# Kernel optimization log

Measured on AMD Instinct MI355X. Metric: run time of the kernel, lower is better.

The kernel has to match this reference:

```python
import jax, jax.numpy as jnp
import numpy as np


def setup_inputs() -> dict:
    key = jax.random.key(0)
    k1, k2, k3, k4 = jax.random.split(key, 4)
    B, S, IN, H = 4, 2048, 512, 1024
    x = jax.random.normal(k1, (B, S, IN), dtype=jnp.float32)
    W1 = jax.random.normal(k2, (IN, H), dtype=jnp.float32) * (1.0 / np.sqrt(IN))
    b1 = jax.random.normal(k3, (H,), dtype=jnp.float32) * 0.02
    Wq = jax.random.normal(k4, (H, H), dtype=jnp.float32) * (1.0 / np.sqrt(H))
    return {"x": x, "W1": W1, "b1": b1, "Wq": Wq, "atten_size": 16}


def reference(x, W1, b1, Wq, atten_size):
    A = atten_size
    B, S, _ = x.shape
    H = W1.shape[1]
    h = jax.nn.relu(jnp.einsum('bsi,ih->bsh', x, W1) + b1)  # [B,S,H]
    # zero-pad sequence dim by A on each side
    padded = jnp.pad(h, ((0, 0), (A, A), (0, 0)))  # [B,S+2A,H]
    # torch: stack(roll(padded, k, 1) for k in -A..A, dim=2) then slice [A:-A]
    # => x_nei[b, i, j] = padded[b, 2A + i - j]
    idx = 2 * A + jnp.arange(S)[:, None] - jnp.arange(2 * A + 1)[None, :]  # [S,W]
    x_nei = padded[:, idx, :]  # [B,S,W,H]
    q = jnp.einsum('bsh,hk->bsk', h, Wq)  # [B,S,H]
    scores = jnp.einsum('bsh,bswh->bsw', q, x_nei) / jnp.sqrt(jnp.asarray(H, x.dtype))
    w = jax.nn.softmax(scores, axis=2)  # softmax over window axis
    out = jnp.einsum('bsw,bswh->bsh', w, x_nei)
    return out
```

## Files before the change

kernel.cpp:

```cpp
#include <hip/hip_runtime.h>
#include <stdint.h>

constexpr int BATCH = 4;
constexpr int SEQ   = 2048;
constexpr int DIN   = 512;
constexpr int DH    = 1024;
constexpr int BS    = BATCH * SEQ;
constexpr int AP    = 32;
constexpr int AW    = 64;

typedef float  floatx4 __attribute__((ext_vector_type(4)));
typedef short  bf16x8  __attribute__((ext_vector_type(8)));

static __device__ __forceinline__ unsigned short f2bf(float f) {
  union { float f; unsigned u; } v; v.f = f;
  unsigned r = (v.u + 0x7fffu + ((v.u >> 16) & 1u)) >> 16;
  return (unsigned short)r;
}

static __device__ __forceinline__ void gld_lds16(const unsigned short* g, const short* l) {
  typedef const __attribute__((address_space(1))) void* gvp;
  typedef __attribute__((address_space(3))) void* lvp;
  __builtin_amdgcn_global_load_lds((gvp)(uintptr_t)g, (lvp)(unsigned)(uintptr_t)l, 16, 0, 0);
}

__global__ __launch_bounds__(256) void transpose_w_k(const float* __restrict__ W1,
                                                     const float* __restrict__ Wq,
                                                     unsigned short* __restrict__ w1t,
                                                     unsigned short* __restrict__ wqt) {
  __shared__ float t[32][33];
  const bool isW1 = blockIdx.y < 16;
  const float* in = isW1 ? W1 : Wq;
  unsigned short* out = isW1 ? w1t : wqt;
  const int R = isW1 ? DIN : DH;
  const int C = DH;
  const int r0 = (isW1 ? blockIdx.y : (blockIdx.y - 16)) * 32;
  const int c0 = blockIdx.x * 32;
  const int tx = threadIdx.x & 31, ty = threadIdx.x >> 5;
  for (int i = ty; i < 32; i += 8) t[i][tx] = in[(size_t)(r0 + i) * C + c0 + tx];
  __syncthreads();
  for (int i = ty; i < 32; i += 8) out[(size_t)(c0 + i) * R + r0 + tx] = f2bf(t[tx][i]);
}

__global__ __launch_bounds__(256) void gemm1_k(const float* __restrict__ X,
                                               const unsigned short* __restrict__ Bt,
                                               const float* __restrict__ bias,
                                               unsigned short* __restrict__ outB,
                                               unsigned short* __restrict__ outBT) {
  const int M = BS, N = DH, K = DIN;
  __shared__ __align__(16) short As0[128 * 32], As1[128 * 32];
  __shared__ __align__(16) short Bs0[128 * 32], Bs1[128 * 32];
  const int tid  = threadIdx.x;
  const int m0   = blockIdx.x * 128, n0 = blockIdx.y * 128;
  const int wv   = tid >> 6, lane = tid & 63;
  const int wm   = (wv >> 1) * 64, wn = (wv & 1) * 64;
  const int l16  = lane & 15, quad = lane >> 4;

  const int ar = tid >> 1, acol = (tid & 1) * 16;
  const float* gX = X + (size_t)(m0 + ar) * K + acol;
  short* lA0 = &As0[ar * 32 + acol];
  short* lA1 = &As1[ar * 32 + acol];
  const int ra = lane >> 2, ca = (lane & 3) * 8;
  const unsigned short* gB = Bt + (size_t)(n0 + wv * 32 + ra) * K + ca;
  const short* lB0a = &Bs0[wv * 1024];
  const short* lB0b = &Bs0[wv * 1024 + 512];
  const short* lB1a = &Bs1[wv * 1024];
  const short* lB1b = &Bs1[wv * 1024 + 512];

  floatx4 acc[4][4];
  for (int i = 0; i < 4; i++)
    for (int j = 0; j < 4; j++) acc[i][j] = {0.f, 0.f, 0.f, 0.f};

  for (int ks = 0; ks < K / 64; ++ks) {
    float4 x0 = ((const float4*)gX)[0], x1 = ((const float4*)gX)[1];
    float4 x2 = ((const float4*)gX)[2], x3 = ((const float4*)gX)[3];
    float4 x4 = ((const float4*)(gX + 32))[0], x5 = ((const float4*)(gX + 32))[1];
    float4 x6 = ((const float4*)(gX + 32))[2], x7 = ((const float4*)(gX + 32))[3];
    gX += 64;
    __align__(16) unsigned short c0[16], c1[16];
    c0[0] = f2bf(x0.x); c0[1] = f2bf(x0.y); c0[2]  = f2bf(x0.z); c0[3]  = f2bf(x0.w);
    c0[4] = f2bf(x1.x); c0[5] = f2bf(x1.y); c0[6]  = f2bf(x1.z); c0[7]  = f2bf(x1.w);
    c0[8] = f2bf(x2.x); c0[9] = f2bf(x2.y); c0[10] = f2bf(x2.z); c0[11] = f2bf(x2.w);
    c0[12] = f2bf(x3.x); c0[13] = f2bf(x3.y); c0[14] = f2bf(x3.z); c0[15] = f2bf(x3.w);
    c1[0] = f2bf(x4.x); c1[1] = f2bf(x4.y); c1[2]  = f2bf(x4.z); c1[3]  = f2bf(x4.w);
    c1[4] = f2bf(x5.x); c1[5] = f2bf(x5.y); c1[6]  = f2bf(x5.z); c1[7]  = f2bf(x5.w);
    c1[8] = f2bf(x6.x); c1[9] = f2bf(x6.y); c1[10] = f2bf(x6.z); c1[11] = f2bf(x6.w);
    c1[12] = f2bf(x7.x); c1[13] = f2bf(x7.y); c1[14] = f2bf(x7.z); c1[15] = f2bf(x7.w);
    __syncthreads();
    gld_lds16(gB, lB0a); gld_lds16(gB + 16 * K, lB0b);
    gld_lds16(gB + 32, lB1a); gld_lds16(gB + 16 * K + 32, lB1b);
    gB += 64;
    ((uint4*)lA0)[0] = ((uint4*)c0)[0];
    ((uint4*)lA0)[1] = ((uint4*)c0)[1];
    ((uint4*)lA1)[0] = ((uint4*)c1)[0];
    ((uint4*)lA1)[1] = ((uint4*)c1)[1];
    __syncthreads();
    bf16x8 af[4], bfr[4];
    for (int i = 0; i < 4; i++)
      af[i] = *(const bf16x8*)&As0[(wm + i * 16 + l16) * 32 + quad * 8];
    for (int j = 0; j < 4; j++)
      bfr[j] = *(const bf16x8*)&Bs0[(wn + j * 16 + l16) * 32 + quad * 8];
    for (int i = 0; i < 4; i++)
      for (int j = 0; j < 4; j++)
        acc[i][j] = __builtin_amdgcn_mfma_f32_16x16x32_bf16(af[i], bfr[j], acc[i][j], 0, 0, 0);
    for (int i = 0; i < 4; i++)
      af[i] = *(const bf16x8*)&As1[(wm + i * 16 + l16) * 32 + quad * 8];
    for (int j = 0; j < 4; j++)
      bfr[j] = *(const bf16x8*)&Bs1[(wn + j * 16 + l16) * 32 + quad * 8];
    for (int i = 0; i < 4; i++)
      for (int j = 0; j < 4; j++)
        acc[i][j] = __builtin_amdgcn_mfma_f32_16x16x32_bf16(af[i], bfr[j], acc[i][j], 0, 0, 0);
  }

  for (int j = 0; j < 4; j++) {
    const int col = n0 + wn + j * 16 + l16;
    const float bv = bias[col];
    for (int i = 0; i < 4; i++) {
      const int rowb = m0 + wm + i * 16 + quad * 4;
      float v[4];
      for (int r = 0; r < 4; r++) v[r] = fmaxf(acc[i][j][r] + bv, 0.f);
      for (int r = 0; r < 4; r++) outB[(size_t)(rowb + r) * N + col] = f2bf(v[r]);
      ushort4 o4; o4.x = f2bf(v[0]); o4.y = f2bf(v[1]); o4.z = f2bf(v[2]); o4.w = f2bf(v[3]);
      *(ushort4*)(outBT + (size_t)col * M + rowb) = o4;
    }
  }
}

__global__ __launch_bounds__(256) void gemm2_k(const unsigned short* __restrict__ Ab,
                                               const unsigned short* __restrict__ Bt,
                                               unsigned short* __restrict__ outB) {
  const int N = DH, K = DH;
  __shared__ __align__(16) short As0[128 * 32], As1[128 * 32];
  __shared__ __align__(16) short Bs0[128 * 32], Bs1[128 * 32];
  const int tid  = threadIdx.x;
  const int m0   = blockIdx.x * 128, n0 = blockIdx.y * 128;
  const int wv   = tid >> 6, lane = tid & 63;
  const int wm   = (wv >> 1) * 64, wn = (wv & 1) * 64;
  const int l16  = lane & 15, quad = lane >> 4;

  const int ra = lane >> 2, ca = (lane & 3) * 8;
  const unsigned short* gA = Ab + (size_t)(m0 + wv * 32 + ra) * K + ca;
  const unsigned short* gB = Bt + (size_t)(n0 + wv * 32 + ra) * K + ca;
  const short* lA0a = &As0[wv * 1024];
  const short* lA0b = &As0[wv * 1024 + 512];
  const short* lA1a = &As1[wv * 1024];
  const short* lA1b = &As1[wv * 1024 + 512];
  const short* lB0a = &Bs0[wv * 1024];
  const short* lB0b = &Bs0[wv * 1024 + 512];
  const short* lB1a = &Bs1[wv * 1024];
  const short* lB1b = &Bs1[wv * 1024 + 512];

  floatx4 acc[4][4];
  for (int i = 0; i < 4; i++)
    for (int j = 0; j < 4; j++) acc[i][j] = {0.f, 0.f, 0.f, 0.f};

  for (int ks = 0; ks < K / 64; ++ks) {
    __syncthreads();
    gld_lds16(gA, lA0a); gld_lds16(gA + 16 * K, lA0b);
    gld_lds16(gA + 32, lA1a); gld_lds16(gA + 16 * K + 32, lA1b);
    gld_lds16(gB, lB0a); gld_lds16(gB + 16 * K, lB0b);
    gld_lds16(gB + 32, lB1a); gld_lds16(gB + 16 * K + 32, lB1b);
    gA += 64; gB += 64;
    __syncthreads();
    bf16x8 af[4], bfr[4];
    for (int i = 0; i < 4; i++)
      af[i] = *(const bf16x8*)&As0[(wm + i * 16 + l16) * 32 + quad * 8];
    for (int j = 0; j < 4; j++)
      bfr[j] = *(const bf16x8*)&Bs0[(wn + j * 16 + l16) * 32 + quad * 8];
    for (int i = 0; i < 4; i++)
      for (int j = 0; j < 4; j++)
        acc[i][j] = __builtin_amdgcn_mfma_f32_16x16x32_bf16(af[i], bfr[j], acc[i][j], 0, 0, 0);
    for (int i = 0; i < 4; i++)
      af[i] = *(const bf16x8*)&As1[(wm + i * 16 + l16) * 32 + quad * 8];
    for (int j = 0; j < 4; j++)
      bfr[j] = *(const bf16x8*)&Bs1[(wn + j * 16 + l16) * 32 + quad * 8];
    for (int i = 0; i < 4; i++)
      for (int j = 0; j < 4; j++)
        acc[i][j] = __builtin_amdgcn_mfma_f32_16x16x32_bf16(af[i], bfr[j], acc[i][j], 0, 0, 0);
  }

  for (int j = 0; j < 4; j++) {
    const int col = n0 + wn + j * 16 + l16;
    for (int i = 0; i < 4; i++) {
      const int rowb = m0 + wm + i * 16 + quad * 4;
      for (int r = 0; r < 4; r++)
        outB[(size_t)(rowb + r) * N + col] = f2bf(acc[i][j][r]);
    }
  }
}

__global__ __launch_bounds__(512) void attn_mfma_k(const unsigned short* __restrict__ hb,
                                                   const unsigned short* __restrict__ hbT,
                                                   const unsigned short* __restrict__ qb,
                                                   float* __restrict__ out) {
  __shared__ float Sf[32 * 64];
  __shared__ __align__(16) short Ps[32 * 72];

  const int tid  = threadIdx.x;
  const int wave = tid >> 6, lane = tid & 63;
  const int l16  = lane & 15, quad = lane >> 4;
  const int p0   = blockIdx.x * AP;
  const int s0   = p0 & (SEQ - 1);

  for (int i = tid; i < 32 * 72 / 2; i += 512) ((unsigned*)Ps)[i] = 0;

  {
    const int mt = wave >> 2, nt = wave & 3;
    const unsigned short* qp = qb + (size_t)(p0 + mt * 16 + l16) * DH + quad * 8;
    const int hrow = s0 - 16 + nt * 16 + l16;
    const bool hv = (hrow >= 0) && (hrow < SEQ);
    const unsigned short* hp = hb + (long long)(p0 - 16 + nt * 16 + l16) * DH + quad * 8;

    floatx4 ac[4] = {{0,0,0,0},{0,0,0,0},{0,0,0,0},{0,0,0,0}};
    const bf16x8 hz = {0,0,0,0,0,0,0,0};
    #pragma unroll
    for (int it = 0; it < 32; ++it) {
      bf16x8 qa = *(const bf16x8*)(qp + it * 32);
      bf16x8 ha = hz;
      if (hv) ha = *(const bf16x8*)(hp + it * 32);
      ac[it & 3] = __builtin_amdgcn_mfma_f32_16x16x32_bf16(qa, ha, ac[it & 3], 0, 0, 0);
    }
    floatx4 s4;
    for (int r = 0; r < 4; r++)
      s4[r] = (ac[0][r] + ac[1][r]) + (ac[2][r] + ac[3][r]);
    for (int r = 0; r < 4; r++)
      Sf[(mt * 16 + quad * 4 + r) * 64 + nt * 16 + l16] = s4[r] * (1.f / 32.f);
  }
  __syncthreads();

  {
    const int row = tid >> 4, k = tid & 15;
    const float v0 = Sf[row * 64 + row + k];
    const float v1 = Sf[row * 64 + row + k + 16];
    const float v2 = (k == 0) ? Sf[row * 64 + row + 32] : -1e30f;
    float mx = fmaxf(v0, fmaxf(v1, v2));
    for (int off = 1; off < 16; off <<= 1) mx = fmaxf(mx, __shfl_xor(mx, off, 64));
    const float e0 = __expf(v0 - mx), e1 = __expf(v1 - mx);
    const float e2 = (k == 0) ? __expf(v2 - mx) : 0.f;
    float sum = e0 + e1 + e2;
    for (int off = 1; off < 16; off <<= 1) sum += __shfl_xor(sum, off, 64);
    const float inv = 1.f / sum;
    Ps[row * 72 + row + k] = f2bf(e0 * inv);
    Ps[row * 72 + row + k + 16] = f2bf(e1 * inv);
    if (k == 0) Ps[row * 72 + row + 32] = f2bf(e2 * inv);
  }
  __syncthreads();

  {
    const bf16x8 pb00 = *(const bf16x8*)&Ps[(l16) * 72 + quad * 8];
    const bf16x8 pb01 = *(const bf16x8*)&Ps[(l16) * 72 + 32 + quad * 8];
    const bf16x8 pb10 = *(const bf16x8*)&Ps[(16 + l16) * 72 + quad * 8];
    const bf16x8 pb11 = *(const bf16x8*)&Ps[(16 + l16) * 72 + 32 + quad * 8];

    int lo = 16 - s0; if (lo < 0) lo = 0;
    int hi = SEQ + 16 - s0; if (hi > AW) hi = AW;
    const bool interior = (lo == 0) && (hi == AW);

    #pragma unroll
    for (int i = 0; i < 8; ++i) {
      const int mt2 = wave * 8 + i;
      const unsigned short* ap = hbT + (size_t)(mt2 * 16 + l16) * BS + (p0 - 16) + quad * 8;
      bf16x8 aa0 = *(const bf16x8*)(ap);
      bf16x8 aa1 = *(const bf16x8*)(ap + 32);
      if (!interior) {
        #pragma unroll
        for (int j = 0; j < 8; j++) {
          const int k = quad * 8 + j;
          if (k < lo || k >= hi) aa0[j] = 0;
          if (k + 32 < lo || k + 32 >= hi) aa1[j] = 0;
        }
      }
      floatx4 o0 = {0.f, 0.f, 0.f, 0.f}, o1 = {0.f, 0.f, 0.f, 0.f};
      o0 = __builtin_amdgcn_mfma_f32_16x16x32_bf16(aa0, pb00, o0, 0, 0, 0);
      o0 = __builtin_amdgcn_mfma_f32_16x16x32_bf16(aa1, pb01, o0, 0, 0, 0);
      o1 = __builtin_amdgcn_mfma_f32_16x16x32_bf16(aa0, pb10, o1, 0, 0, 0);
      o1 = __builtin_amdgcn_mfma_f32_16x16x32_bf16(aa1, pb11, o1, 0, 0, 0);
      float4 s0v; s0v.x = o0[0]; s0v.y = o0[1]; s0v.z = o0[2]; s0v.w = o0[3];
      float4 s1v; s1v.x = o1[0]; s1v.y = o1[1]; s1v.z = o1[2]; s1v.w = o1[3];
      *(float4*)(out + (size_t)(p0 + l16) * DH + mt2 * 16 + quad * 4) = s0v;
      *(float4*)(out + (size_t)(p0 + 16 + l16) * DH + mt2 * 16 + quad * 4) = s1v;
    }
  }
}

extern "C" void kernel_launch(void* const* d_in, const int* in_sizes, int n_in,
                              void* d_out, int out_size, void* d_ws, size_t ws_size,
                              hipStream_t stream) {
  const float* x  = (const float*)d_in[0];
  const float* W1 = (const float*)d_in[1];
  const float* b1 = (const float*)d_in[2];
  const float* Wq = (const float*)d_in[3];

  char* w = (char*)d_ws;
  unsigned short* w1t = (unsigned short*)(w);
  unsigned short* wqt = (unsigned short*)(w + (1ull  << 20));
  unsigned short* hb  = (unsigned short*)(w + (3ull  << 20));
  unsigned short* hbT = (unsigned short*)(w + (19ull << 20));
  unsigned short* qb  = (unsigned short*)(w + (35ull << 20));

  transpose_w_k<<<dim3(DH / 32, 48), 256, 0, stream>>>(W1, Wq, w1t, wqt);

  gemm1_k<<<dim3(BS / 128, DH / 128), 256, 0, stream>>>(x, w1t, b1, hb, hbT);
  gemm2_k<<<dim3(BS / 128, DH / 128), 256, 0, stream>>>(hb, wqt, qb);

  attn_mfma_k<<<BS / AP, 512, 0, stream>>>(hb, hbT, qb, (float*)d_out);
}
```

Baseline: 157.7 us.

## Fuse Q projection GEMM into attention kernel, drop separate gemm2 pass

Removes the standalone h·Wq GEMM kernel and computes each block's 32 rows of q inside the attention kernel. Each wave computes a 32x128 strip of q with MFMA, reading A and B operands straight from global memory, then stages it through LDS in two halves for the score computation. This avoids writing q to global memory and reading it back, and saves one kernel launch. In exchange every attention block reads all of Wq without LDS tiling, and the q computation has low arithmetic reuse, so it relies on L2 hits for Wq.

```diff
diff --git a/kernel.cpp b/kernel.cpp
--- a/kernel.cpp
+++ b/kernel.cpp
@@ -8,6 +8,7 @@
 constexpr int BS    = BATCH * SEQ;
 constexpr int AP    = 32;
 constexpr int AW    = 64;
+constexpr int QS    = 524;
 
 typedef float  floatx4 __attribute__((ext_vector_type(4)));
 typedef short  bf16x8  __attribute__((ext_vector_type(8)));
@@ -126,73 +127,11 @@
   }
 }
 
-__global__ __launch_bounds__(256) void gemm2_k(const unsigned short* __restrict__ Ab,
-                                               const unsigned short* __restrict__ Bt,
-                                               unsigned short* __restrict__ outB) {
-  const int N = DH, K = DH;
-  __shared__ __align__(16) short As0[128 * 32], As1[128 * 32];
-  __shared__ __align__(16) short Bs0[128 * 32], Bs1[128 * 32];
-  const int tid  = threadIdx.x;
-  const int m0   = blockIdx.x * 128, n0 = blockIdx.y * 128;
-  const int wv   = tid >> 6, lane = tid & 63;
-  const int wm   = (wv >> 1) * 64, wn = (wv & 1) * 64;
-  const int l16  = lane & 15, quad = lane >> 4;
-
-  const int ra = lane >> 2, ca = (lane & 3) * 8;
-  const unsigned short* gA = Ab + (size_t)(m0 + wv * 32 + ra) * K + ca;
-  const unsigned short* gB = Bt + (size_t)(n0 + wv * 32 + ra) * K + ca;
-  const short* lA0a = &As0[wv * 1024];
-  const short* lA0b = &As0[wv * 1024 + 512];
-  const short* lA1a = &As1[wv * 1024];
-  const short* lA1b = &As1[wv * 1024 + 512];
-  const short* lB0a = &Bs0[wv * 1024];
-  const short* lB0b = &Bs0[wv * 1024 + 512];
-  const short* lB1a = &Bs1[wv * 1024];
-  const short* lB1b = &Bs1[wv * 1024 + 512];
-
-  floatx4 acc[4][4];
-  for (int i = 0; i < 4; i++)
-    for (int j = 0; j < 4; j++) acc[i][j] = {0.f, 0.f, 0.f, 0.f};
-
-  for (int ks = 0; ks < K / 64; ++ks) {
-    __syncthreads();
-    gld_lds16(gA, lA0a); gld_lds16(gA + 16 * K, lA0b);
-    gld_lds16(gA + 32, lA1a); gld_lds16(gA + 16 * K + 32, lA1b);
-    gld_lds16(gB, lB0a); gld_lds16(gB + 16 * K, lB0b);
-    gld_lds16(gB + 32, lB1a); gld_lds16(gB + 16 * K + 32, lB1b);
-    gA += 64; gB += 64;
-    __syncthreads();
-    bf16x8 af[4], bfr[4];
-    for (int i = 0; i < 4; i++)
-      af[i] = *(const bf16x8*)&As0[(wm + i * 16 + l16) * 32 + quad * 8];
-    for (int j = 0; j < 4; j++)
-      bfr[j] = *(const bf16x8*)&Bs0[(wn + j * 16 + l16) * 32 + quad * 8];
-    for (int i = 0; i < 4; i++)
-      for (int j = 0; j < 4; j++)
-        acc[i][j] = __builtin_amdgcn_mfma_f32_16x16x32_bf16(af[i], bfr[j], acc[i][j], 0, 0, 0);
-    for (int i = 0; i < 4; i++)
-      af[i] = *(const bf16x8*)&As1[(wm + i * 16 + l16) * 32 + quad * 8];
-    for (int j = 0; j < 4; j++)
-      bfr[j] = *(const bf16x8*)&Bs1[(wn + j * 16 + l16) * 32 + quad * 8];
-    for (int i = 0; i < 4; i++)
-      for (int j = 0; j < 4; j++)
-        acc[i][j] = __builtin_amdgcn_mfma_f32_16x16x32_bf16(af[i], bfr[j], acc[i][j], 0, 0, 0);
-  }
-
-  for (int j = 0; j < 4; j++) {
-    const int col = n0 + wn + j * 16 + l16;
-    for (int i = 0; i < 4; i++) {
-      const int rowb = m0 + wm + i * 16 + quad * 4;
-      for (int r = 0; r < 4; r++)
-        outB[(size_t)(rowb + r) * N + col] = f2bf(acc[i][j][r]);
-    }
-  }
-}
-
-__global__ __launch_bounds__(512) void attn_mfma_k(const unsigned short* __restrict__ hb,
-                                                   const unsigned short* __restrict__ hbT,
-                                                   const unsigned short* __restrict__ qb,
-                                                   float* __restrict__ out) {
+__global__ __launch_bounds__(512) void attn_fused_k(const unsigned short* __restrict__ hb,
+                                                    const unsigned short* __restrict__ hbT,
+                                                    const unsigned short* __restrict__ wqt,
+                                                    float* __restrict__ out) {
+  __shared__ __align__(16) short Qs[32 * QS];
   __shared__ float Sf[32 * 64];
   __shared__ __align__(16) short Ps[32 * 72];
 
@@ -204,22 +143,54 @@
 
   for (int i = tid; i < 32 * 72 / 2; i += 512) ((unsigned*)Ps)[i] = 0;
 
-  {
-    const int mt = wave >> 2, nt = wave & 3;
-    const unsigned short* qp = qb + (size_t)(p0 + mt * 16 + l16) * DH + quad * 8;
-    const int hrow = s0 - 16 + nt * 16 + l16;
-    const bool hv = (hrow >= 0) && (hrow < SEQ);
-    const unsigned short* hp = hb + (long long)(p0 - 16 + nt * 16 + l16) * DH + quad * 8;
-
-    floatx4 ac[4] = {{0,0,0,0},{0,0,0,0},{0,0,0,0},{0,0,0,0}};
-    const bf16x8 hz = {0,0,0,0,0,0,0,0};
+  floatx4 qacc[2][8];
+  for (int i = 0; i < 2; i++)
+    for (int j = 0; j < 8; j++) qacc[i][j] = {0.f, 0.f, 0.f, 0.f};
+  {
+    const unsigned short* ga0 = hb + (size_t)(p0 + l16) * DH + quad * 8;
+    const unsigned short* ga1 = hb + (size_t)(p0 + 16 + l16) * DH + quad * 8;
+    const unsigned short* gb  = wqt + (size_t)(wave * 128 + l16) * DH + quad * 8;
+    for (int kb = 0; kb < 32; ++kb) {
+      const int ko = kb * 32;
+      bf16x8 a0 = *(const bf16x8*)(ga0 + ko);
+      bf16x8 a1 = *(const bf16x8*)(ga1 + ko);
+      #pragma unroll
+      for (int nt = 0; nt < 8; ++nt) {
+        bf16x8 b = *(const bf16x8*)(gb + (size_t)nt * 16 * DH + ko);
+        qacc[0][nt] = __builtin_amdgcn_mfma_f32_16x16x32_bf16(a0, b, qacc[0][nt], 0, 0, 0);
+        qacc[1][nt] = __builtin_amdgcn_mfma_f32_16x16x32_bf16(a1, b, qacc[1][nt], 0, 0, 0);
+      }
+    }
+  }
+
+  const int mt = wave >> 2, nt = wave & 3;
+  const int hrow = s0 - 16 + nt * 16 + l16;
+  const bool hv = (hrow >= 0) && (hrow < SEQ);
+  const unsigned short* hp = hb + (long long)(p0 - 16 + nt * 16 + l16) * DH + quad * 8;
+  floatx4 ac[4] = {{0,0,0,0},{0,0,0,0},{0,0,0,0},{0,0,0,0}};
+  const bf16x8 hz = {0,0,0,0,0,0,0,0};
+
+  #pragma unroll
+  for (int half = 0; half < 2; ++half) {
+    if ((wave >> 2) == half) {
+      const int strip = (wave & 3) * 128;
+      for (int m2 = 0; m2 < 2; m2++)
+        for (int n2 = 0; n2 < 8; n2++)
+          for (int r = 0; r < 4; r++)
+            Qs[(m2 * 16 + quad * 4 + r) * QS + strip + n2 * 16 + l16] =
+                f2bf(qacc[m2][n2][r]);
+    }
+    __syncthreads();
     #pragma unroll
-    for (int it = 0; it < 32; ++it) {
-      bf16x8 qa = *(const bf16x8*)(qp + it * 32);
+    for (int it = 0; it < 16; ++it) {
+      bf16x8 qa = *(const bf16x8*)&Qs[(mt * 16 + l16) * QS + it * 32 + quad * 8];
       bf16x8 ha = hz;
-      if (hv) ha = *(const bf16x8*)(hp + it * 32);
+      if (hv) ha = *(const bf16x8*)(hp + half * 512 + it * 32);
       ac[it & 3] = __builtin_amdgcn_mfma_f32_16x16x32_bf16(qa, ha, ac[it & 3], 0, 0, 0);
     }
+    __syncthreads();
+  }
+  {
     floatx4 s4;
     for (int r = 0; r < 4; r++)
       s4[r] = (ac[0][r] + ac[1][r]) + (ac[2][r] + ac[3][r]);
@@ -296,12 +267,10 @@
   unsigned short* wqt = (unsigned short*)(w + (1ull  << 20));
   unsigned short* hb  = (unsigned short*)(w + (3ull  << 20));
   unsigned short* hbT = (unsigned short*)(w + (19ull << 20));
-  unsigned short* qb  = (unsigned short*)(w + (35ull << 20));
 
   transpose_w_k<<<dim3(DH / 32, 48), 256, 0, stream>>>(W1, Wq, w1t, wqt);
 
   gemm1_k<<<dim3(BS / 128, DH / 128), 256, 0, stream>>>(x, w1t, b1, hb, hbT);
-  gemm2_k<<<dim3(BS / 128, DH / 128), 256, 0, stream>>>(hb, wqt, qb);
-
-  attn_mfma_k<<<BS / AP, 512, 0, stream>>>(hb, hbT, qb, (float*)d_out);
-}
+
+  attn_fused_k<<<BS / AP, 512, 0, stream>>>(hb, hbT, wqt, (float*)d_out);
+}
```

Result: slower. 200.7 us (+27.3%).
